# Kernel tuning notes

Hardware: AMD Instinct MI355X
Metric: run time of the kernel (lower is better)

The kernel has to match this reference:

```python
import jax, jax.numpy as jnp
import numpy as np

EPSILON = 1e-8
DAMPING = 0.7
B, PREV, SIZE, NXT = 8192, 2000, 2000, 2000


def standardize(x):
    # per-sample standardization over features (torch.std uses ddof=1)
    mean = x.mean(axis=1, keepdims=True)
    std = jnp.std(x, axis=1, ddof=1, keepdims=True)
    return (x - mean) / (std + EPSILON)


def setup_inputs() -> dict:
    key = jax.random.key(0)
    ks = jax.random.split(key, 9)
    return {
        "prev_act": jax.random.normal(ks[0], (B, PREV), jnp.float32),
        "self_act": jax.random.normal(ks[1], (B, SIZE), jnp.float32),
        "next_act": jax.random.normal(ks[2], (B, NXT), jnp.float32),
        "forward_W": jax.random.normal(ks[3], (SIZE, PREV), jnp.float32) * 0.02,
        "forward_b": jax.random.normal(ks[4], (SIZE,), jnp.float32) * 0.02,
        "backward_W": jax.random.normal(ks[5], (SIZE, NXT), jnp.float32) * 0.02,
        "backward_b": jax.random.normal(ks[6], (SIZE,), jnp.float32) * 0.02,
        "lateral_W": jax.random.normal(ks[7], (SIZE, SIZE), jnp.float32) * 0.02,
        "lateral_b": jax.random.normal(ks[8], (SIZE,), jnp.float32) * 0.02,
    }


def reference(prev_act, self_act, next_act, forward_W, forward_b,
              backward_W, backward_b, lateral_W, lateral_b):
    # middle HiddenLayer forward: fwd(prev) + next.backward(next) + lateral(self)
    prev_s = standardize(prev_act)   # [B, PREV]
    next_s = standardize(next_act)   # [B, NXT]
    self_s = standardize(self_act)   # [B, SIZE]
    pre = (jnp.einsum('bp,sp->bs', prev_s, forward_W) + forward_b
           + jnp.einsum('bn,sn->bs', next_s, backward_W) + backward_b
           + jnp.einsum('bk,sk->bs', self_s, lateral_W) + lateral_b)
    new_act = jax.nn.relu(pre)
    # damped recurrent update
    return DAMPING * new_act + (1.0 - DAMPING) * self_act
```

## Files before the change

### kernel.cpp

```cpp
#include <hip/hip_runtime.h>
#include <hip/hip_bf16.h>

constexpr int BATCH = 8192;
constexpr int NREAL = 2000;
constexpr int KSLOT = 2048;
constexpr int KPAD  = 6144;
constexpr int NPAD  = 2048;
constexpr int NT    = KPAD / 64;

typedef short bf16x8 __attribute__((ext_vector_type(8)));
typedef float f32x4  __attribute__((ext_vector_type(4)));

__device__ inline void gload_lds16(const void* g, void* l) {
  __builtin_amdgcn_global_load_lds(
      (const __attribute__((address_space(1))) unsigned int*)g,
      (__attribute__((address_space(3))) unsigned int*)l,
      16, 0, 0);
}

__device__ inline unsigned short f2bf(float x) {
  union { float f; unsigned int u; } v;
  v.f = x;
  unsigned int r = v.u + 0x7fffu + ((v.u >> 16) & 1u);
  return (unsigned short)(r >> 16);
}

__global__ __launch_bounds__(256) void std_pack_kernel(
    const float* __restrict__ prev, const float* __restrict__ nxt,
    const float* __restrict__ selfa, unsigned short* __restrict__ Acat) {
  __shared__ float red[4];
  const int row = blockIdx.x;
  const int mat = blockIdx.y;
  const float* src = (mat == 0) ? prev : (mat == 1) ? nxt : selfa;
  const int t = threadIdx.x;

  float x[8];
  float s1 = 0.f;
  if (t < 250) {
    const float4* p = (const float4*)(src + (size_t)row * NREAL + t * 8);
    float4 a = p[0], b = p[1];
    x[0] = a.x; x[1] = a.y; x[2] = a.z; x[3] = a.w;
    x[4] = b.x; x[5] = b.y; x[6] = b.z; x[7] = b.w;
#pragma unroll
    for (int j = 0; j < 8; ++j) s1 += x[j];
  } else {
#pragma unroll
    for (int j = 0; j < 8; ++j) x[j] = 0.f;
  }
#pragma unroll
  for (int o = 32; o; o >>= 1) s1 += __shfl_xor(s1, o);
  if ((t & 63) == 0) red[t >> 6] = s1;
  __syncthreads();
  const float mean = (red[0] + red[1] + red[2] + red[3]) * (1.f / 2000.f);
  __syncthreads();

  float ss = 0.f;
  if (t < 250) {
#pragma unroll
    for (int j = 0; j < 8; ++j) { float d = x[j] - mean; ss += d * d; }
  }
#pragma unroll
  for (int o = 32; o; o >>= 1) ss += __shfl_xor(ss, o);
  if ((t & 63) == 0) red[t >> 6] = ss;
  __syncthreads();
  const float var = (red[0] + red[1] + red[2] + red[3]) * (1.f / 1999.f);
  const float scale = 1.f / (sqrtf(var) + 1e-8f);

  unsigned short o8[8];
  if (t < 250) {
#pragma unroll
    for (int j = 0; j < 8; ++j) o8[j] = f2bf((x[j] - mean) * scale);
  } else {
#pragma unroll
    for (int j = 0; j < 8; ++j) o8[j] = 0;
  }
  uint4 q;
  q.x = (unsigned)o8[0] | ((unsigned)o8[1] << 16);
  q.y = (unsigned)o8[2] | ((unsigned)o8[3] << 16);
  q.z = (unsigned)o8[4] | ((unsigned)o8[5] << 16);
  q.w = (unsigned)o8[6] | ((unsigned)o8[7] << 16);
  *(uint4*)(Acat + (size_t)row * KPAD + mat * KSLOT + t * 8) = q;
}

__global__ __launch_bounds__(256) void w_pack_kernel(
    const float* __restrict__ fW, const float* __restrict__ bW,
    const float* __restrict__ lW, unsigned short* __restrict__ Wcat) {
  const int s = blockIdx.x;
  const int mat = blockIdx.y;
  const int t = threadIdx.x;
  uint4 q = make_uint4(0, 0, 0, 0);
  if (s < NREAL && t < 250) {
    const float* src = ((mat == 0) ? fW : (mat == 1) ? bW : lW) +
                       (size_t)s * NREAL + t * 8;
    const float4* p = (const float4*)src;
    float4 a = p[0], b = p[1];
    q.x = (unsigned)f2bf(a.x) | ((unsigned)f2bf(a.y) << 16);
    q.y = (unsigned)f2bf(a.z) | ((unsigned)f2bf(a.w) << 16);
    q.z = (unsigned)f2bf(b.x) | ((unsigned)f2bf(b.y) << 16);
    q.w = (unsigned)f2bf(b.z) | ((unsigned)f2bf(b.w) << 16);
  }
  *(uint4*)(Wcat + (size_t)s * KPAD + mat * KSLOT + t * 8) = q;
}

__global__ __launch_bounds__(512, 2) void gemm_kernel(
    const unsigned short* __restrict__ A,
    const unsigned short* __restrict__ W,
    const float* __restrict__ fb, const float* __restrict__ bb,
    const float* __restrict__ lb,
    const float* __restrict__ selfact,
    float* __restrict__ out) {
  __shared__ unsigned short lds[2][2][2][256][32];
  unsigned short* ldsF = &lds[0][0][0][0][0];

  const int tid  = threadIdx.x;
  const int wave = tid >> 6;
  const int lane = tid & 63;
  const int wm = wave >> 2;
  const int wn = wave & 3;

  const int nbid = (blockIdx.x & 7) * 32 + (blockIdx.x >> 3);
  const int bm = nbid >> 3;
  const int bn = nbid & 7;

  const int srow = tid >> 2;
  const int sc = (tid & 3) ^ ((srow >> 1) & 3);
  const unsigned short* Asrc =
      A + (size_t)(bm * 256 + srow) * KPAD + sc * 8;
  const unsigned short* Bsrc =
      W + (size_t)(bn * 256 + srow) * KPAD + sc * 8;

  const int pcx = (lane >> 4) ^ ((lane >> 1) & 3);
  const unsigned short* aF = ldsF + (wm * 128 + (lane & 15)) * 32 + pcx * 8;
  const unsigned short* bF = ldsF + (wn * 64 + (lane & 15)) * 32 + pcx * 8;

  f32x4 acc[8][4] = {};
  bf16x8 bf[4];

#define STAGE(sb, mat, h, tt) { \
    const unsigned short* g_ = ((mat) ? Bsrc : Asrc) + (size_t)(tt) * 64 + (h) * 32; \
    unsigned short* d_ = ldsF + ((sb) * 4 + (mat) * 2 + (h)) * 8192 + wave * 64 * 8; \
    gload_lds16(g_, d_); \
    gload_lds16(g_ + (size_t)128 * KPAD, d_ + 512 * 8); \
  }

#define MFMA16(mh) \
    _Pragma("unroll") for (int fm = 0; fm < 4; ++fm) \
    _Pragma("unroll") for (int fn = 0; fn < 4; ++fn) \
      acc[(mh) * 4 + fm][fn] = __builtin_amdgcn_mfma_f32_16x16x32_bf16( \
          af[fm], bf[fn], acc[(mh) * 4 + fm][fn], 0, 0, 0);

#define PHASE(b, kk, mh, STG, VM) { \
    bf16x8 af[4]; \
    _Pragma("unroll") for (int fm = 0; fm < 4; ++fm) \
      af[fm] = *(const bf16x8*)(aF + ((b) * 4 + (kk)) * 8192 + ((mh) * 64 + fm * 16) * 32); \
    if ((mh) == 0) { \
      _Pragma("unroll") for (int fn = 0; fn < 4; ++fn) \
        bf[fn] = *(const bf16x8*)(bF + ((b) * 4 + 2 + (kk)) * 8192 + (fn * 16) * 32); \
    } \
    STG \
    __builtin_amdgcn_s_barrier(); \
    __builtin_amdgcn_s_setprio(1); \
    MFMA16(mh) \
    __builtin_amdgcn_s_setprio(0); \
    asm volatile("s_waitcnt vmcnt(" VM ")"); \
    __builtin_amdgcn_s_barrier(); \
  }

#define TILE(t, b, VM) { \
    PHASE(b, 0, 0, if ((t) + 1 < NT) STAGE(((b) ^ 1), 0, 1, (t) + 1);, VM) \
    PHASE(b, 0, 1, if ((t) + 1 < NT) STAGE(((b) ^ 1), 1, 1, (t) + 1);, VM) \
    PHASE(b, 1, 0, if ((t) + 2 < NT) STAGE((b), 0, 0, (t) + 2);, VM) \
    PHASE(b, 1, 1, if ((t) + 2 < NT) STAGE((b), 1, 0, (t) + 2);, VM) \
  }

  STAGE(0, 0, 0, 0)
  STAGE(0, 1, 0, 0)
  STAGE(0, 0, 1, 0)
  STAGE(0, 1, 1, 0)
  STAGE(1, 0, 0, 1)
  STAGE(1, 1, 0, 1)
  asm volatile("s_waitcnt vmcnt(8)");
  __builtin_amdgcn_s_barrier();

  for (int t = 0; t < NT - 2; ++t) {
    const int b = t & 1;
    TILE(t, b, "6")
  }
  TILE(NT - 2, ((NT - 2) & 1), "0")
  TILE(NT - 1, ((NT - 1) & 1), "0")

  const int colLane = lane & 15;
  const int rowGrp  = (lane >> 4) * 4;
#pragma unroll
  for (int fn = 0; fn < 4; ++fn) {
    const int col = bn * 256 + wn * 64 + fn * 16 + colLane;
    if (col < NREAL) {
      const float bias = fb[col] + bb[col] + lb[col];
#pragma unroll
      for (int m = 0; m < 8; ++m) {
        const int row0 = bm * 256 + wm * 128 + m * 16 + rowGrp;
#pragma unroll
        for (int r = 0; r < 4; ++r) {
          const float pre = acc[m][fn][r] + bias;
          const size_t oi = (size_t)(row0 + r) * NREAL + col;
          out[oi] = 0.7f * fmaxf(pre, 0.f) + 0.3f * selfact[oi];
        }
      }
    }
  }
#undef TILE
#undef PHASE
#undef MFMA16
#undef STAGE
}

extern "C" void kernel_launch(void* const* d_in, const int* in_sizes, int n_in,
                              void* d_out, int out_size, void* d_ws,
                              size_t ws_size, hipStream_t stream) {
  const float* prev = (const float*)d_in[0];
  const float* selfa = (const float*)d_in[1];
  const float* nxt  = (const float*)d_in[2];
  const float* fW = (const float*)d_in[3];
  const float* fb = (const float*)d_in[4];
  const float* bW = (const float*)d_in[5];
  const float* bb = (const float*)d_in[6];
  const float* lW = (const float*)d_in[7];
  const float* lb = (const float*)d_in[8];
  float* out = (float*)d_out;

  unsigned short* Acat = (unsigned short*)d_ws;
  unsigned short* Wcat = Acat + (size_t)BATCH * KPAD;

  std_pack_kernel<<<dim3(BATCH, 3), 256, 0, stream>>>(prev, nxt, selfa, Acat);
  w_pack_kernel<<<dim3(NPAD, 3), 256, 0, stream>>>(fW, bW, lW, Wcat);
  gemm_kernel<<<dim3(32 * 8), 512, 0, stream>>>(Acat, Wcat, fb, bb, lb,
                                                selfa, out);
}
```

Before: 277.5 us.

## Software-pipeline LDS fragment reads with MFMA and merge pack kernels

Restructures the GEMM main loop so LDS fragment reads for the next phase are issued into alternate register buffers while the current MFMA block executes, with single-tile global prefetch instead of two-tile lookahead. Also merges activation standardization and weight packing into one launch to cut a kernel launch. The shallower global prefetch may expose memory latency, and the extra fragment registers raise register pressure.

```diff
diff --git a/kernel.cpp b/kernel.cpp
--- a/kernel.cpp
+++ b/kernel.cpp
@@ -25,14 +25,35 @@
   return (unsigned short)(r >> 16);
 }
 
-__global__ __launch_bounds__(256) void std_pack_kernel(
+__global__ __launch_bounds__(256) void pack_kernel(
     const float* __restrict__ prev, const float* __restrict__ nxt,
-    const float* __restrict__ selfa, unsigned short* __restrict__ Acat) {
+    const float* __restrict__ selfa,
+    const float* __restrict__ fW, const float* __restrict__ bW,
+    const float* __restrict__ lW,
+    unsigned short* __restrict__ Acat, unsigned short* __restrict__ Wcat) {
+  const int mat = blockIdx.y;
+  const int t = threadIdx.x;
+
+  if (blockIdx.x >= BATCH) {
+    const int s = blockIdx.x - BATCH;
+    uint4 q = make_uint4(0, 0, 0, 0);
+    if (s < NREAL && t < 250) {
+      const float* src = ((mat == 0) ? fW : (mat == 1) ? bW : lW) +
+                         (size_t)s * NREAL + t * 8;
+      const float4* p = (const float4*)src;
+      float4 a = p[0], b = p[1];
+      q.x = (unsigned)f2bf(a.x) | ((unsigned)f2bf(a.y) << 16);
+      q.y = (unsigned)f2bf(a.z) | ((unsigned)f2bf(a.w) << 16);
+      q.z = (unsigned)f2bf(b.x) | ((unsigned)f2bf(b.y) << 16);
+      q.w = (unsigned)f2bf(b.z) | ((unsigned)f2bf(b.w) << 16);
+    }
+    *(uint4*)(Wcat + (size_t)s * KPAD + mat * KSLOT + t * 8) = q;
+    return;
+  }
+
   __shared__ float red[4];
   const int row = blockIdx.x;
-  const int mat = blockIdx.y;
   const float* src = (mat == 0) ? prev : (mat == 1) ? nxt : selfa;
-  const int t = threadIdx.x;
 
   float x[8];
   float s1 = 0.f;
@@ -80,26 +101,6 @@
   q.z = (unsigned)o8[4] | ((unsigned)o8[5] << 16);
   q.w = (unsigned)o8[6] | ((unsigned)o8[7] << 16);
   *(uint4*)(Acat + (size_t)row * KPAD + mat * KSLOT + t * 8) = q;
-}
-
-__global__ __launch_bounds__(256) void w_pack_kernel(
-    const float* __restrict__ fW, const float* __restrict__ bW,
-    const float* __restrict__ lW, unsigned short* __restrict__ Wcat) {
-  const int s = blockIdx.x;
-  const int mat = blockIdx.y;
-  const int t = threadIdx.x;
-  uint4 q = make_uint4(0, 0, 0, 0);
-  if (s < NREAL && t < 250) {
-    const float* src = ((mat == 0) ? fW : (mat == 1) ? bW : lW) +
-                       (size_t)s * NREAL + t * 8;
-    const float4* p = (const float4*)src;
-    float4 a = p[0], b = p[1];
-    q.x = (unsigned)f2bf(a.x) | ((unsigned)f2bf(a.y) << 16);
-    q.y = (unsigned)f2bf(a.z) | ((unsigned)f2bf(a.w) << 16);
-    q.z = (unsigned)f2bf(b.x) | ((unsigned)f2bf(b.y) << 16);
-    q.w = (unsigned)f2bf(b.z) | ((unsigned)f2bf(b.w) << 16);
-  }
-  *(uint4*)(Wcat + (size_t)s * KPAD + mat * KSLOT + t * 8) = q;
 }
 
 __global__ __launch_bounds__(512, 2) void gemm_kernel(
@@ -134,7 +135,7 @@
   const unsigned short* bF = ldsF + (wn * 64 + (lane & 15)) * 32 + pcx * 8;
 
   f32x4 acc[8][4] = {};
-  bf16x8 bf[4];
+  bf16x8 afA[4], afB[4], bf0[4], bf1[4];
 
 #define STAGE(sb, mat, h, tt) { \
     const unsigned short* g_ = ((mat) ? Bsrc : Asrc) + (size_t)(tt) * 64 + (h) * 32; \
@@ -143,51 +144,63 @@
     gload_lds16(g_ + (size_t)128 * KPAD, d_ + 512 * 8); \
   }
 
-#define MFMA16(mh) \
+#define READ_AF(dst, bb, kk, mh) \
+    _Pragma("unroll") for (int fm = 0; fm < 4; ++fm) \
+      dst[fm] = *(const bf16x8*)(aF + ((bb) * 4 + (kk)) * 8192 + ((mh) * 64 + fm * 16) * 32);
+
+#define READ_BF(dst, bb, kk) \
+    _Pragma("unroll") for (int fn = 0; fn < 4; ++fn) \
+      dst[fn] = *(const bf16x8*)(bF + ((bb) * 4 + 2 + (kk)) * 8192 + (fn * 16) * 32);
+
+#define MFMA16(afr, bfr, mh) { \
+    __builtin_amdgcn_s_setprio(1); \
     _Pragma("unroll") for (int fm = 0; fm < 4; ++fm) \
     _Pragma("unroll") for (int fn = 0; fn < 4; ++fn) \
       acc[(mh) * 4 + fm][fn] = __builtin_amdgcn_mfma_f32_16x16x32_bf16( \
-          af[fm], bf[fn], acc[(mh) * 4 + fm][fn], 0, 0, 0);
-
-#define PHASE(b, kk, mh, STG, VM) { \
-    bf16x8 af[4]; \
-    _Pragma("unroll") for (int fm = 0; fm < 4; ++fm) \
-      af[fm] = *(const bf16x8*)(aF + ((b) * 4 + (kk)) * 8192 + ((mh) * 64 + fm * 16) * 32); \
-    if ((mh) == 0) { \
-      _Pragma("unroll") for (int fn = 0; fn < 4; ++fn) \
-        bf[fn] = *(const bf16x8*)(bF + ((b) * 4 + 2 + (kk)) * 8192 + (fn * 16) * 32); \
-    } \
-    STG \
-    __builtin_amdgcn_s_barrier(); \
-    __builtin_amdgcn_s_setprio(1); \
-    MFMA16(mh) \
+          afr[fm], bfr[fn], acc[(mh) * 4 + fm][fn], 0, 0, 0); \
     __builtin_amdgcn_s_setprio(0); \
-    asm volatile("s_waitcnt vmcnt(" VM ")"); \
-    __builtin_amdgcn_s_barrier(); \
-  }
-
-#define TILE(t, b, VM) { \
-    PHASE(b, 0, 0, if ((t) + 1 < NT) STAGE(((b) ^ 1), 0, 1, (t) + 1);, VM) \
-    PHASE(b, 0, 1, if ((t) + 1 < NT) STAGE(((b) ^ 1), 1, 1, (t) + 1);, VM) \
-    PHASE(b, 1, 0, if ((t) + 2 < NT) STAGE((b), 0, 0, (t) + 2);, VM) \
-    PHASE(b, 1, 1, if ((t) + 2 < NT) STAGE((b), 1, 0, (t) + 2);, VM) \
   }
 
   STAGE(0, 0, 0, 0)
   STAGE(0, 1, 0, 0)
   STAGE(0, 0, 1, 0)
   STAGE(0, 1, 1, 0)
-  STAGE(1, 0, 0, 1)
-  STAGE(1, 1, 0, 1)
-  asm volatile("s_waitcnt vmcnt(8)");
+  asm volatile("s_waitcnt vmcnt(4)" ::: "memory");
   __builtin_amdgcn_s_barrier();
-
-  for (int t = 0; t < NT - 2; ++t) {
+  __builtin_amdgcn_sched_barrier(0);
+  READ_AF(afA, 0, 0, 0)
+  READ_BF(bf0, 0, 0)
+
+  for (int t = 0; t < NT; ++t) {
     const int b = t & 1;
-    TILE(t, b, "6")
-  }
-  TILE(NT - 2, ((NT - 2) & 1), "0")
-  TILE(NT - 1, ((NT - 1) & 1), "0")
+    const bool pf = (t + 1 < NT);
+    __builtin_amdgcn_s_barrier();
+    __builtin_amdgcn_sched_barrier(0);
+    READ_AF(afB, b, 0, 1)
+    if (pf) STAGE(b ^ 1, 0, 0, t + 1)
+    MFMA16(afA, bf0, 0)
+    asm volatile("s_waitcnt vmcnt(2)" ::: "memory");
+    __builtin_amdgcn_s_barrier();
+    __builtin_amdgcn_sched_barrier(0);
+    READ_AF(afA, b, 1, 0)
+    READ_BF(bf1, b, 1)
+    if (pf) STAGE(b ^ 1, 1, 0, t + 1)
+    MFMA16(afB, bf0, 1)
+    __builtin_amdgcn_s_barrier();
+    __builtin_amdgcn_sched_barrier(0);
+    READ_AF(afB, b, 1, 1)
+    if (pf) STAGE(b ^ 1, 0, 1, t + 1)
+    MFMA16(afA, bf1, 0)
+    asm volatile("s_waitcnt vmcnt(2)" ::: "memory");
+    __builtin_amdgcn_s_barrier();
+    __builtin_amdgcn_sched_barrier(0);
+    if (pf) {
+      READ_AF(afA, b ^ 1, 0, 0)
+      READ_BF(bf0, b ^ 1, 0)
+      STAGE(b ^ 1, 1, 1, t + 1)
+    }
+    MFMA16(afB, bf1, 1)
+  }
 
   const int colLane = lane & 15;
   const int rowGrp  = (lane >> 4) * 4;
@@ -208,9 +221,9 @@
       }
     }
   }
-#undef TILE
-#undef PHASE
 #undef MFMA16
+#undef READ_BF
+#undef READ_AF
 #undef STAGE
 }
 
@@ -231,8 +244,8 @@
   unsigned short* Acat = (unsigned short*)d_ws;
   unsigned short* Wcat = Acat + (size_t)BATCH * KPAD;
 
-  std_pack_kernel<<<dim3(BATCH, 3), 256, 0, stream>>>(prev, nxt, selfa, Acat);
-  w_pack_kernel<<<dim3(NPAD, 3), 256, 0, stream>>>(fW, bW, lW, Wcat);
+  pack_kernel<<<dim3(BATCH + NPAD, 3), 256, 0, stream>>>(
+      prev, nxt, selfa, fW, bW, lW, Acat, Wcat);
   gemm_kernel<<<dim3(32 * 8), 512, 0, stream>>>(Acat, Wcat, fb, bb, lb,
                                                 selfa, out);
 }
```

Result: faster. 267.5 us (-3.6%).

## Merge pack kernels and restructure GEMM main loop into four row-split phases

Applied to the files above, without the earlier changes.

The two packing kernels are merged into one launch, with extra blocks along the grid handling the weight conversion, which removes a launch and lets activation and weight packing overlap. The GEMM main loop is reorganised so each phase covers two 16-row A fragments across the full K=64 step with all B fragments loaded once per tile. Global-to-LDS staging is split into quarter-sized loads spread across the four phases, and LDS waits are made explicit with lgkmcnt. The swizzle index is also changed to depend on tid bits, and the loop is manually unrolled by two tiles. This adds careful vmcnt accounting with a higher risk of race conditions.

```diff
diff --git a/kernel.cpp b/kernel.cpp
--- a/kernel.cpp
+++ b/kernel.cpp
@@ -25,14 +25,35 @@
   return (unsigned short)(r >> 16);
 }
 
-__global__ __launch_bounds__(256) void std_pack_kernel(
+__global__ __launch_bounds__(256) void pack_kernel(
     const float* __restrict__ prev, const float* __restrict__ nxt,
-    const float* __restrict__ selfa, unsigned short* __restrict__ Acat) {
+    const float* __restrict__ selfa,
+    const float* __restrict__ fW, const float* __restrict__ bW,
+    const float* __restrict__ lW,
+    unsigned short* __restrict__ Acat, unsigned short* __restrict__ Wcat) {
+  const int mat = blockIdx.y;
+  const int t = threadIdx.x;
+
+  if (blockIdx.x >= BATCH) {
+    const int s = blockIdx.x - BATCH;
+    uint4 q = make_uint4(0, 0, 0, 0);
+    if (s < NREAL && t < 250) {
+      const float* src = ((mat == 0) ? fW : (mat == 1) ? bW : lW) +
+                         (size_t)s * NREAL + t * 8;
+      const float4* p = (const float4*)src;
+      float4 a = p[0], b = p[1];
+      q.x = (unsigned)f2bf(a.x) | ((unsigned)f2bf(a.y) << 16);
+      q.y = (unsigned)f2bf(a.z) | ((unsigned)f2bf(a.w) << 16);
+      q.z = (unsigned)f2bf(b.x) | ((unsigned)f2bf(b.y) << 16);
+      q.w = (unsigned)f2bf(b.z) | ((unsigned)f2bf(b.w) << 16);
+    }
+    *(uint4*)(Wcat + (size_t)s * KPAD + mat * KSLOT + t * 8) = q;
+    return;
+  }
+
   __shared__ float red[4];
   const int row = blockIdx.x;
-  const int mat = blockIdx.y;
   const float* src = (mat == 0) ? prev : (mat == 1) ? nxt : selfa;
-  const int t = threadIdx.x;
 
   float x[8];
   float s1 = 0.f;
@@ -82,26 +103,6 @@
   *(uint4*)(Acat + (size_t)row * KPAD + mat * KSLOT + t * 8) = q;
 }
 
-__global__ __launch_bounds__(256) void w_pack_kernel(
-    const float* __restrict__ fW, const float* __restrict__ bW,
-    const float* __restrict__ lW, unsigned short* __restrict__ Wcat) {
-  const int s = blockIdx.x;
-  const int mat = blockIdx.y;
-  const int t = threadIdx.x;
-  uint4 q = make_uint4(0, 0, 0, 0);
-  if (s < NREAL && t < 250) {
-    const float* src = ((mat == 0) ? fW : (mat == 1) ? bW : lW) +
-                       (size_t)s * NREAL + t * 8;
-    const float4* p = (const float4*)src;
-    float4 a = p[0], b = p[1];
-    q.x = (unsigned)f2bf(a.x) | ((unsigned)f2bf(a.y) << 16);
-    q.y = (unsigned)f2bf(a.z) | ((unsigned)f2bf(a.w) << 16);
-    q.z = (unsigned)f2bf(b.x) | ((unsigned)f2bf(b.y) << 16);
-    q.w = (unsigned)f2bf(b.z) | ((unsigned)f2bf(b.w) << 16);
-  }
-  *(uint4*)(Wcat + (size_t)s * KPAD + mat * KSLOT + t * 8) = q;
-}
-
 __global__ __launch_bounds__(512, 2) void gemm_kernel(
     const unsigned short* __restrict__ A,
     const unsigned short* __restrict__ W,
@@ -109,8 +110,8 @@
     const float* __restrict__ lb,
     const float* __restrict__ selfact,
     float* __restrict__ out) {
-  __shared__ unsigned short lds[2][2][2][256][32];
-  unsigned short* ldsF = &lds[0][0][0][0][0];
+  __shared__ unsigned short ldsS[2][2][2][256][32];
+  unsigned short* ldsF = &ldsS[0][0][0][0][0];
 
   const int tid  = threadIdx.x;
   const int wave = tid >> 6;
@@ -123,7 +124,7 @@
   const int bn = nbid & 7;
 
   const int srow = tid >> 2;
-  const int sc = (tid & 3) ^ ((srow >> 1) & 3);
+  const int sc = (tid & 3) ^ ((tid >> 3) & 3);
   const unsigned short* Asrc =
       A + (size_t)(bm * 256 + srow) * KPAD + sc * 8;
   const unsigned short* Bsrc =
@@ -134,60 +135,73 @@
   const unsigned short* bF = ldsF + (wn * 64 + (lane & 15)) * 32 + pcx * 8;
 
   f32x4 acc[8][4] = {};
-  bf16x8 bf[4];
-
-#define STAGE(sb, mat, h, tt) { \
-    const unsigned short* g_ = ((mat) ? Bsrc : Asrc) + (size_t)(tt) * 64 + (h) * 32; \
-    unsigned short* d_ = ldsF + ((sb) * 4 + (mat) * 2 + (h)) * 8192 + wave * 64 * 8; \
+  bf16x8 bfr[4][2];
+
+#define STQ(bu, mat, kq, rh, tt) { \
+    const unsigned short* g_ = ((mat) ? Bsrc : Asrc) + \
+        (size_t)(rh) * 128 * KPAD + (size_t)(tt) * 64 + (kq) * 32; \
+    unsigned short* d_ = ldsF + ((bu) * 4 + (mat) * 2 + (kq)) * 8192 + \
+        (rh) * 4096 + wave * 512; \
     gload_lds16(g_, d_); \
-    gload_lds16(g_ + (size_t)128 * KPAD, d_ + 512 * 8); \
-  }
-
-#define MFMA16(mh) \
-    _Pragma("unroll") for (int fm = 0; fm < 4; ++fm) \
+  }
+
+#define READ_BF(bu) \
     _Pragma("unroll") for (int fn = 0; fn < 4; ++fn) \
-      acc[(mh) * 4 + fm][fn] = __builtin_amdgcn_mfma_f32_16x16x32_bf16( \
-          af[fm], bf[fn], acc[(mh) * 4 + fm][fn], 0, 0, 0);
-
-#define PHASE(b, kk, mh, STG, VM) { \
-    bf16x8 af[4]; \
-    _Pragma("unroll") for (int fm = 0; fm < 4; ++fm) \
-      af[fm] = *(const bf16x8*)(aF + ((b) * 4 + (kk)) * 8192 + ((mh) * 64 + fm * 16) * 32); \
-    if ((mh) == 0) { \
-      _Pragma("unroll") for (int fn = 0; fn < 4; ++fn) \
-        bf[fn] = *(const bf16x8*)(bF + ((b) * 4 + 2 + (kk)) * 8192 + (fn * 16) * 32); \
+    _Pragma("unroll") for (int kk = 0; kk < 2; ++kk) \
+      bfr[fn][kk] = *(const bf16x8*)(bF + ((bu) * 4 + 2 + kk) * 8192 + fn * 512);
+
+#define PHASE(bu, p, STG, GATE) { \
+    bf16x8 a00 = *(const bf16x8*)(aF + ((bu) * 4 + 0) * 8192 + (2 * (p)) * 512); \
+    bf16x8 a01 = *(const bf16x8*)(aF + ((bu) * 4 + 1) * 8192 + (2 * (p)) * 512); \
+    bf16x8 a10 = *(const bf16x8*)(aF + ((bu) * 4 + 0) * 8192 + (2 * (p) + 1) * 512); \
+    bf16x8 a11 = *(const bf16x8*)(aF + ((bu) * 4 + 1) * 8192 + (2 * (p) + 1) * 512); \
+    if ((p) == 0) { READ_BF(bu) } \
+    STG \
+    if ((p) == 0) asm volatile("s_waitcnt lgkmcnt(8)" ::: "memory"); \
+    __builtin_amdgcn_s_barrier(); \
+    asm volatile("s_waitcnt lgkmcnt(0)" ::: "memory"); \
+    __builtin_amdgcn_s_setprio(1); \
+    _Pragma("unroll") for (int fn = 0; fn < 4; ++fn) { \
+      acc[2 * (p)][fn] = __builtin_amdgcn_mfma_f32_16x16x32_bf16( \
+          a00, bfr[fn][0], acc[2 * (p)][fn], 0, 0, 0); \
+      acc[2 * (p)][fn] = __builtin_amdgcn_mfma_f32_16x16x32_bf16( \
+          a01, bfr[fn][1], acc[2 * (p)][fn], 0, 0, 0); \
+      acc[2 * (p) + 1][fn] = __builtin_amdgcn_mfma_f32_16x16x32_bf16( \
+          a10, bfr[fn][0], acc[2 * (p) + 1][fn], 0, 0, 0); \
+      acc[2 * (p) + 1][fn] = __builtin_amdgcn_mfma_f32_16x16x32_bf16( \
+          a11, bfr[fn][1], acc[2 * (p) + 1][fn], 0, 0, 0); \
     } \
-    STG \
+    __builtin_amdgcn_s_setprio(0); \
+    GATE \
     __builtin_amdgcn_s_barrier(); \
-    __builtin_amdgcn_s_setprio(1); \
-    MFMA16(mh) \
-    __builtin_amdgcn_s_setprio(0); \
-    asm volatile("s_waitcnt vmcnt(" VM ")"); \
-    __builtin_amdgcn_s_barrier(); \
-  }
-
-#define TILE(t, b, VM) { \
-    PHASE(b, 0, 0, if ((t) + 1 < NT) STAGE(((b) ^ 1), 0, 1, (t) + 1);, VM) \
-    PHASE(b, 0, 1, if ((t) + 1 < NT) STAGE(((b) ^ 1), 1, 1, (t) + 1);, VM) \
-    PHASE(b, 1, 0, if ((t) + 2 < NT) STAGE((b), 0, 0, (t) + 2);, VM) \
-    PHASE(b, 1, 1, if ((t) + 2 < NT) STAGE((b), 1, 0, (t) + 2);, VM) \
-  }
-
-  STAGE(0, 0, 0, 0)
-  STAGE(0, 1, 0, 0)
-  STAGE(0, 0, 1, 0)
-  STAGE(0, 1, 1, 0)
-  STAGE(1, 0, 0, 1)
-  STAGE(1, 1, 0, 1)
-  asm volatile("s_waitcnt vmcnt(8)");
+  }
+
+#define TILE(bu, t, SA, SB, GATE) { \
+    PHASE(bu, 0, if (SA) { STQ((bu) ^ 1, 0, 0, 0, (t) + 1) STQ((bu) ^ 1, 0, 1, 0, (t) + 1) }, ) \
+    PHASE(bu, 1, if (SA) { STQ((bu) ^ 1, 0, 0, 1, (t) + 1) STQ((bu) ^ 1, 0, 1, 1, (t) + 1) }, ) \
+    PHASE(bu, 2, if (SB) { STQ((bu), 1, 0, 0, (t) + 2) STQ((bu), 1, 1, 0, (t) + 2) }, ) \
+    PHASE(bu, 3, if (SB) { STQ((bu), 1, 0, 1, (t) + 2) STQ((bu), 1, 1, 1, (t) + 2) }, GATE) \
+  }
+
+  STQ(0, 0, 0, 0, 0) STQ(0, 0, 1, 0, 0)
+  STQ(0, 0, 0, 1, 0) STQ(0, 0, 1, 1, 0)
+  STQ(0, 1, 0, 0, 0) STQ(0, 1, 1, 0, 0)
+  STQ(0, 1, 0, 1, 0) STQ(0, 1, 1, 1, 0)
+  STQ(1, 1, 0, 0, 1) STQ(1, 1, 1, 0, 1)
+  STQ(1, 1, 0, 1, 1) STQ(1, 1, 1, 1, 1)
+  asm volatile("s_waitcnt vmcnt(4)" ::: "memory");
   __builtin_amdgcn_s_barrier();
 
-  for (int t = 0; t < NT - 2; ++t) {
-    const int b = t & 1;
-    TILE(t, b, "6")
-  }
-  TILE(NT - 2, ((NT - 2) & 1), "0")
-  TILE(NT - 1, ((NT - 1) & 1), "0")
+  for (int i = 0; i < 47; ++i) {
+    const int t = 2 * i;
+    TILE(0, t, true, true,
+         asm volatile("s_waitcnt vmcnt(4)" ::: "memory");)
+    TILE(1, t + 1, true, true,
+         asm volatile("s_waitcnt vmcnt(4)" ::: "memory");)
+  }
+  TILE(0, 94, true, false,
+       asm volatile("s_waitcnt vmcnt(0)" ::: "memory");)
+  TILE(1, 95, false, false, )
 
   const int colLane = lane & 15;
   const int rowGrp  = (lane >> 4) * 4;
@@ -197,11 +211,11 @@
     if (col < NREAL) {
       const float bias = fb[col] + bb[col] + lb[col];
 #pragma unroll
-      for (int m = 0; m < 8; ++m) {
-        const int row0 = bm * 256 + wm * 128 + m * 16 + rowGrp;
+      for (int fm = 0; fm < 8; ++fm) {
+        const int row0 = bm * 256 + wm * 128 + fm * 16 + rowGrp;
 #pragma unroll
         for (int r = 0; r < 4; ++r) {
-          const float pre = acc[m][fn][r] + bias;
+          const float pre = acc[fm][fn][r] + bias;
           const size_t oi = (size_t)(row0 + r) * NREAL + col;
           out[oi] = 0.7f * fmaxf(pre, 0.f) + 0.3f * selfact[oi];
         }
@@ -210,8 +224,8 @@
   }
 #undef TILE
 #undef PHASE
-#undef MFMA16
-#undef STAGE
+#undef READ_BF
+#undef STQ
 }
 
 extern "C" void kernel_launch(void* const* d_in, const int* in_sizes, int n_in,
@@ -231,8 +245,8 @@
   unsigned short* Acat = (unsigned short*)d_ws;
   unsigned short* Wcat = Acat + (size_t)BATCH * KPAD;
 
-  std_pack_kernel<<<dim3(BATCH, 3), 256, 0, stream>>>(prev, nxt, selfa, Acat);
-  w_pack_kernel<<<dim3(NPAD, 3), 256, 0, stream>>>(fW, bW, lW, Wcat);
+  pack_kernel<<<dim3(BATCH + NPAD, 3), 256, 0, stream>>>(
+      prev, nxt, selfa, fW, bW, lW, Acat, Wcat);
   gemm_kernel<<<dim3(32 * 8), 512, 0, stream>>>(Acat, Wcat, fb, bb, lb,
                                                 selfa, out);
 }
```

After: 255.5 us (median of 2 runs). -7.9%, faster.

## Pre-pack weights into MFMA fragment layout and load B directly to registers

Applied to the files above, without the earlier changes.

The weight pack kernel now writes W in a fragment-ordered layout, so each lane's bf16x8 MFMA operand is contiguous. The GEMM no longer stages W through LDS: it loads B fragments straight from global into double-buffered registers and keeps only A in LDS. The main loop changes from four barrier-separated phases per K-tile to one block per K-tile with a full vmcnt(0) wait. This cuts LDS traffic and the LDS footprint, but adds register pressure and exposes global-load latency for B.

```diff
diff --git a/kernel.cpp b/kernel.cpp
--- a/kernel.cpp
+++ b/kernel.cpp
@@ -25,7 +25,7 @@
   return (unsigned short)(r >> 16);
 }
 
-__global__ __launch_bounds__(256) void std_pack_kernel(
+__global__ __launch_bounds__(256) void apack_kernel(
     const float* __restrict__ prev, const float* __restrict__ nxt,
     const float* __restrict__ selfa, unsigned short* __restrict__ Acat) {
   __shared__ float red[4];
@@ -82,35 +82,53 @@
   *(uint4*)(Acat + (size_t)row * KPAD + mat * KSLOT + t * 8) = q;
 }
 
-__global__ __launch_bounds__(256) void w_pack_kernel(
+__global__ __launch_bounds__(256) void wfrag_kernel(
     const float* __restrict__ fW, const float* __restrict__ bW,
-    const float* __restrict__ lW, unsigned short* __restrict__ Wcat) {
-  const int s = blockIdx.x;
-  const int mat = blockIdx.y;
+    const float* __restrict__ lW, unsigned short* __restrict__ Wfr) {
+  __shared__ unsigned short tile[16][520];
+  const int cb16 = blockIdx.x;
+  const int m = blockIdx.y;
+  const float* src = (m == 0) ? fW : (m == 1) ? bW : lW;
   const int t = threadIdx.x;
-  uint4 q = make_uint4(0, 0, 0, 0);
-  if (s < NREAL && t < 250) {
-    const float* src = ((mat == 0) ? fW : (mat == 1) ? bW : lW) +
-                       (size_t)s * NREAL + t * 8;
-    const float4* p = (const float4*)src;
-    float4 a = p[0], b = p[1];
-    q.x = (unsigned)f2bf(a.x) | ((unsigned)f2bf(a.y) << 16);
-    q.y = (unsigned)f2bf(a.z) | ((unsigned)f2bf(a.w) << 16);
-    q.z = (unsigned)f2bf(b.x) | ((unsigned)f2bf(b.y) << 16);
-    q.w = (unsigned)f2bf(b.z) | ((unsigned)f2bf(b.w) << 16);
-  }
-  *(uint4*)(Wcat + (size_t)s * KPAD + mat * KSLOT + t * 8) = q;
+  const int r = t >> 4;
+  const int c = t & 15;
+  const int s = cb16 * 16 + r;
+  const bool rowok = (s < NREAL);
+
+  for (int kc0 = 0; kc0 < KSLOT; kc0 += 512) {
+#pragma unroll
+    for (int v = 0; v < 8; ++v) {
+      const int k = kc0 + c * 32 + v * 4;
+      float4 f = make_float4(0.f, 0.f, 0.f, 0.f);
+      if (rowok && k < NREAL)
+        f = *(const float4*)(src + (size_t)s * NREAL + k);
+      tile[r][c * 32 + v * 4 + 0] = f2bf(f.x);
+      tile[r][c * 32 + v * 4 + 1] = f2bf(f.y);
+      tile[r][c * 32 + v * 4 + 2] = f2bf(f.z);
+      tile[r][c * 32 + v * 4 + 3] = f2bf(f.w);
+    }
+    __syncthreads();
+#pragma unroll
+    for (int w = 0; w < 4; ++w) {
+      const int slot = w * 4 + (t >> 6);
+      const int lane = t & 63;
+      const uint4 q = *(const uint4*)&tile[lane & 15][slot * 32 + (lane >> 4) * 8];
+      *(uint4*)(Wfr + ((size_t)(cb16 * 192 + m * 64 + (kc0 >> 5) + slot) * 512)
+                + lane * 8) = q;
+    }
+    __syncthreads();
+  }
 }
 
 __global__ __launch_bounds__(512, 2) void gemm_kernel(
     const unsigned short* __restrict__ A,
-    const unsigned short* __restrict__ W,
+    const unsigned short* __restrict__ Wfr,
     const float* __restrict__ fb, const float* __restrict__ bb,
     const float* __restrict__ lb,
     const float* __restrict__ selfact,
     float* __restrict__ out) {
-  __shared__ unsigned short lds[2][2][2][256][32];
-  unsigned short* ldsF = &lds[0][0][0][0][0];
+  __shared__ unsigned short ldsA[2][2][8192];
+  unsigned short* ldsF = &ldsA[0][0][0];
 
   const int tid  = threadIdx.x;
   const int wave = tid >> 6;
@@ -123,71 +141,66 @@
   const int bn = nbid & 7;
 
   const int srow = tid >> 2;
-  const int sc = (tid & 3) ^ ((srow >> 1) & 3);
+  const int sc = (tid & 3) ^ ((tid >> 3) & 3);
   const unsigned short* Asrc =
       A + (size_t)(bm * 256 + srow) * KPAD + sc * 8;
-  const unsigned short* Bsrc =
-      W + (size_t)(bn * 256 + srow) * KPAD + sc * 8;
 
   const int pcx = (lane >> 4) ^ ((lane >> 1) & 3);
   const unsigned short* aF = ldsF + (wm * 128 + (lane & 15)) * 32 + pcx * 8;
-  const unsigned short* bF = ldsF + (wn * 64 + (lane & 15)) * 32 + pcx * 8;
+
+  const unsigned short* Bbase =
+      Wfr + (size_t)(bn * 16 + wn * 4) * 192 * 512 + lane * 8;
 
   f32x4 acc[8][4] = {};
-  bf16x8 bf[4];
-
-#define STAGE(sb, mat, h, tt) { \
-    const unsigned short* g_ = ((mat) ? Bsrc : Asrc) + (size_t)(tt) * 64 + (h) * 32; \
-    unsigned short* d_ = ldsF + ((sb) * 4 + (mat) * 2 + (h)) * 8192 + wave * 64 * 8; \
+  bf16x8 bcA[4][2], bcB[4][2];
+
+#define STQ(bu, kq, rh, tt) { \
+    const unsigned short* g_ = Asrc + (size_t)(rh) * 128 * KPAD + \
+        (size_t)(tt) * 64 + (kq) * 32; \
+    unsigned short* d_ = ldsF + ((bu) * 2 + (kq)) * 8192 + (rh) * 4096 + \
+        wave * 512; \
     gload_lds16(g_, d_); \
-    gload_lds16(g_ + (size_t)128 * KPAD, d_ + 512 * 8); \
-  }
-
-#define MFMA16(mh) \
-    _Pragma("unroll") for (int fm = 0; fm < 4; ++fm) \
+  }
+#define STAGE_A(bu, tt) { \
+    STQ(bu, 0, 0, tt) STQ(bu, 0, 1, tt) STQ(bu, 1, 0, tt) STQ(bu, 1, 1, tt) }
+
+#define LOADB(dst, tt) \
     _Pragma("unroll") for (int fn = 0; fn < 4; ++fn) \
-      acc[(mh) * 4 + fm][fn] = __builtin_amdgcn_mfma_f32_16x16x32_bf16( \
-          af[fm], bf[fn], acc[(mh) * 4 + fm][fn], 0, 0, 0);
-
-#define PHASE(b, kk, mh, STG, VM) { \
-    bf16x8 af[4]; \
-    _Pragma("unroll") for (int fm = 0; fm < 4; ++fm) \
-      af[fm] = *(const bf16x8*)(aF + ((b) * 4 + (kk)) * 8192 + ((mh) * 64 + fm * 16) * 32); \
-    if ((mh) == 0) { \
-      _Pragma("unroll") for (int fn = 0; fn < 4; ++fn) \
-        bf[fn] = *(const bf16x8*)(bF + ((b) * 4 + 2 + (kk)) * 8192 + (fn * 16) * 32); \
+    _Pragma("unroll") for (int kq = 0; kq < 2; ++kq) \
+      dst[fn][kq] = *(const bf16x8*)(Bbase + (size_t)fn * 98304 + \
+          ((size_t)(tt) * 2 + kq) * 512);
+
+#define TILEB(q, tt, bcur, bnxt, DOB, DOST) { \
+    if (DOB) { LOADB(bnxt, (tt) + 1) } \
+    if (DOST) { STAGE_A((q) ^ 1, (tt) + 1) } \
+    _Pragma("unroll") for (int kk = 0; kk < 2; ++kk) { \
+      __builtin_amdgcn_s_setprio(1); \
+      _Pragma("unroll") for (int fm = 0; fm < 8; ++fm) { \
+        bf16x8 af = *(const bf16x8*)(aF + ((q) * 2 + kk) * 8192 + fm * 512); \
+        _Pragma("unroll") for (int fn = 0; fn < 4; ++fn) \
+          acc[fm][fn] = __builtin_amdgcn_mfma_f32_16x16x32_bf16( \
+              af, bcur[fn][kk], acc[fm][fn], 0, 0, 0); \
+      } \
+      __builtin_amdgcn_s_setprio(0); \
     } \
-    STG \
+    asm volatile("s_waitcnt vmcnt(0)" ::: "memory"); \
     __builtin_amdgcn_s_barrier(); \
-    __builtin_amdgcn_s_setprio(1); \
-    MFMA16(mh) \
-    __builtin_amdgcn_s_setprio(0); \
-    asm volatile("s_waitcnt vmcnt(" VM ")"); \
-    __builtin_amdgcn_s_barrier(); \
-  }
-
-#define TILE(t, b, VM) { \
-    PHASE(b, 0, 0, if ((t) + 1 < NT) STAGE(((b) ^ 1), 0, 1, (t) + 1);, VM) \
-    PHASE(b, 0, 1, if ((t) + 1 < NT) STAGE(((b) ^ 1), 1, 1, (t) + 1);, VM) \
-    PHASE(b, 1, 0, if ((t) + 2 < NT) STAGE((b), 0, 0, (t) + 2);, VM) \
-    PHASE(b, 1, 1, if ((t) + 2 < NT) STAGE((b), 1, 0, (t) + 2);, VM) \
-  }
-
-  STAGE(0, 0, 0, 0)
-  STAGE(0, 1, 0, 0)
-  STAGE(0, 0, 1, 0)
-  STAGE(0, 1, 1, 0)
-  STAGE(1, 0, 0, 1)
-  STAGE(1, 1, 0, 1)
-  asm volatile("s_waitcnt vmcnt(8)");
+    __builtin_amdgcn_sched_barrier(0); \
+  }
+
+  STAGE_A(0, 0)
+  LOADB(bcA, 0)
+  asm volatile("s_waitcnt vmcnt(0)" ::: "memory");
   __builtin_amdgcn_s_barrier();
-
-  for (int t = 0; t < NT - 2; ++t) {
-    const int b = t & 1;
-    TILE(t, b, "6")
-  }
-  TILE(NT - 2, ((NT - 2) & 1), "0")
-  TILE(NT - 1, ((NT - 1) & 1), "0")
+  __builtin_amdgcn_sched_barrier(0);
+
+  for (int i = 0; i < 47; ++i) {
+    const int t = 2 * i;
+    TILEB(0, t, bcA, bcB, true, true)
+    TILEB(1, t + 1, bcB, bcA, true, true)
+  }
+  TILEB(0, 94, bcA, bcB, true, true)
+  TILEB(1, 95, bcB, bcA, false, false)
 
   const int colLane = lane & 15;
   const int rowGrp  = (lane >> 4) * 4;
@@ -197,21 +210,21 @@
     if (col < NREAL) {
       const float bias = fb[col] + bb[col] + lb[col];
 #pragma unroll
-      for (int m = 0; m < 8; ++m) {
-        const int row0 = bm * 256 + wm * 128 + m * 16 + rowGrp;
+      for (int fm = 0; fm < 8; ++fm) {
+        const int row0 = bm * 256 + wm * 128 + fm * 16 + rowGrp;
 #pragma unroll
         for (int r = 0; r < 4; ++r) {
-          const float pre = acc[m][fn][r] + bias;
+          const float pre = acc[fm][fn][r] + bias;
           const size_t oi = (size_t)(row0 + r) * NREAL + col;
           out[oi] = 0.7f * fmaxf(pre, 0.f) + 0.3f * selfact[oi];
         }
       }
     }
   }
-#undef TILE
-#undef PHASE
-#undef MFMA16
-#undef STAGE
+#undef TILEB
+#undef LOADB
+#undef STAGE_A
+#undef STQ
 }
 
 extern "C" void kernel_launch(void* const* d_in, const int* in_sizes, int n_in,
@@ -229,10 +242,10 @@
   float* out = (float*)d_out;
 
   unsigned short* Acat = (unsigned short*)d_ws;
-  unsigned short* Wcat = Acat + (size_t)BATCH * KPAD;
-
-  std_pack_kernel<<<dim3(BATCH, 3), 256, 0, stream>>>(prev, nxt, selfa, Acat);
-  w_pack_kernel<<<dim3(NPAD, 3), 256, 0, stream>>>(fW, bW, lW, Wcat);
-  gemm_kernel<<<dim3(32 * 8), 512, 0, stream>>>(Acat, Wcat, fb, bb, lb,
+  unsigned short* Wfr  = Acat + (size_t)BATCH * KPAD;
+
+  apack_kernel<<<dim3(BATCH, 3), 256, 0, stream>>>(prev, nxt, selfa, Acat);
+  wfrag_kernel<<<dim3(128, 3), 256, 0, stream>>>(fW, bW, lW, Wfr);
+  gemm_kernel<<<dim3(32 * 8), 512, 0, stream>>>(Acat, Wfr, fb, bb, lb,
                                                 selfa, out);
 }
```

New measurement: 317.5 us. 1.14x slower.
